# Performance work log

Measured on AMD Instinct MI355X. Metric: run time of the kernel, lower is better.

## Reference

```python
import jax, jax.numpy as jnp
import numpy as np

L, P, B, C, H, W = 2, 2, 4, 128, 64, 64
K = 2  # negatives per sample


def setup_inputs() -> dict:
    key = jax.random.key(0)
    k1, k2, k3, k4, k5 = jax.random.split(key, 5)
    shp = (L, P, B, C, H, W)
    return {
        "style_E": jax.random.normal(k1, shp, dtype=jnp.float32),
        "style_S": jax.random.normal(k2, shp, dtype=jnp.float32),
        "translate_E": jax.random.normal(k3, shp, dtype=jnp.float32),
        "translate_S": jax.random.normal(k4, shp, dtype=jnp.float32),
        "neg_idx": jax.random.randint(k5, (B, K), 0, B, dtype=jnp.int32),
    }


def reference(style_E, style_S, translate_E, translate_S, neg_idx):
    # Stack E and S levels: [2L, P, B, C, N] with N = H*W
    S = jnp.concatenate([style_E, style_S], axis=0).reshape(2 * L, P, B, C, -1)
    T = jnp.concatenate([translate_E, translate_S], axis=0).reshape(2 * L, P, B, C, -1)

    # EFDM: sort style values; permute them to trans's rank order, then MSE.
    Vs = jnp.sort(S, axis=-1)                      # value_style
    idx_t = jnp.argsort(T, axis=-1)                # index_trans
    inv = jnp.argsort(idx_t, axis=-1)              # inverse_index

    # Positive pairs: style[b] vs trans[b]
    matched_pos = jnp.take_along_axis(Vs, inv, axis=-1)
    # mse over (C, N) per slice (matches mse_loss on a [1,C,N] tensor)
    pos = jnp.mean((T - matched_pos) ** 2, axis=(3, 4))  # [2L, P, B]
    poss_loss = pos.sum(axis=(0, 1))                      # [B]

    # Negatives: style[nb] vs trans[b] for nb in neg_idx[b]
    Vs_neg = Vs[:, :, neg_idx]                            # [2L, P, B, K, C, N]
    matched_neg = jnp.take_along_axis(Vs_neg, inv[:, :, :, None], axis=-1)
    neg = jnp.mean((T[:, :, :, None] - matched_neg) ** 2, axis=(4, 5))  # [2L, P, B, K]
    neg_loss = neg.sum(axis=(0, 1, 3))                    # [B]

    return jnp.sum(poss_loss / neg_loss)
```

## Files before the change

### kernel.cpp

```cpp
#include <hip/hip_runtime.h>


typedef unsigned int u32;
typedef __fp16 f16x2 __attribute__((ext_vector_type(2)));

constexpr int N     = 4096;
constexpr int NTH   = 256;
constexpr int CDIM  = 128;
constexpr int BDIM  = 4;
constexpr int KNEG  = 2;
constexpr int ROWS  = 4096;
constexpr int HALF  = 2048;
constexpr int ROWW  = N / 2;
constexpr int LSTRW = 20;
constexpr int LDSW  = NTH * LSTRW;

__device__ inline int lslot(int t) { return t * LSTRW; }

__device__ inline u32 pk_min(u32 a, u32 b) {
  u32 d; asm("v_pk_min_f16 %0, %1, %2" : "=v"(d) : "v"(a), "v"(b)); return d;
}
__device__ inline u32 pk_max(u32 a, u32 b) {
  u32 d; asm("v_pk_max_f16 %0, %1, %2" : "=v"(d) : "v"(a), "v"(b)); return d;
}
__device__ inline u32 pk_min_negb(u32 a, u32 b) {
  u32 d; asm("v_pk_min_f16 %0, %1, %2 neg_lo:[0,1] neg_hi:[0,1]" : "=v"(d) : "v"(a), "v"(b)); return d;
}
__device__ inline u32 pk_sub(u32 a, u32 b) {
  u32 d; asm("v_pk_add_f16 %0, %1, %2 neg_lo:[0,1] neg_hi:[0,1]" : "=v"(d) : "v"(a), "v"(b)); return d;
}
__device__ inline float dot2acc(u32 d, float acc) {
  asm("v_dot2_f32_f16 %0, %1, %2, %0" : "+v"(acc) : "v"(d), "v"(d)); return acc;
}
__device__ inline void pk_cswap(u32& a, u32& b) {
  const u32 mn = pk_min(a, b), mx = pk_max(a, b);
  a = mn; b = mx;
}

template<int CTRL>
__device__ inline u32 dpp_u(u32 x) {
  return (u32)__builtin_amdgcn_update_dpp((int)x, (int)x, CTRL, 0xF, 0xF, false);
}
template<int TM>
__device__ inline u32 dppx(u32 x) {
  if constexpr (TM == 1)      return dpp_u<0xB1>(x);
  else if constexpr (TM == 2) return dpp_u<0x4E>(x);
  else if constexpr (TM == 4)
    return (u32)__builtin_amdgcn_ds_swizzle((int)x, 0x101F);
  else                        return dpp_u<0x128>(x);
}
__device__ inline void swap32u(u32& a, u32& b) {
  asm("v_permlane32_swap_b32 %0, %1" : "+v"(a), "+v"(b));
}
__device__ inline void swap16u(u32& a, u32& b) {
  asm("v_permlane16_swap_b32 %0, %1" : "+v"(a), "+v"(b));
}

__device__ inline void flip16(u32 h[16], u32 f) {
  #pragma unroll
  for (int p = 0; p < 16; ++p) h[p] ^= f;
}

struct PolM { u32 s1, s2, s4, s8; };

template<int TM>
__device__ inline void polar_pass16(u32 h[16]) {
  #pragma unroll
  for (int g = 0; g < 16; g += 8) {
    u32 o[8];
    #pragma unroll
    for (int p = 0; p < 8; ++p) o[p] = dppx<TM>(h[g + p]);
    #pragma unroll
    for (int p = 0; p < 8; ++p) h[g + p] = pk_min_negb(h[g + p], o[p]);
  }
}

template<int TMS, bool SKIP_ENTRY>
__device__ inline void polar_block16(u32 h[16], const PolM& pm) {
  if constexpr (!SKIP_ENTRY) {
    const u32 e = (TMS == 8) ? pm.s8 : (TMS == 4) ? pm.s4 : (TMS == 2) ? pm.s2 : pm.s1;
    flip16(h, e);
  }
  if constexpr (TMS >= 8) { polar_pass16<8>(h); flip16(h, pm.s8 ^ pm.s4); }
  if constexpr (TMS >= 4) { polar_pass16<4>(h); flip16(h, pm.s4 ^ pm.s2); }
  if constexpr (TMS >= 2) { polar_pass16<2>(h); flip16(h, pm.s2 ^ pm.s1); }
  polar_pass16<1>(h);
  flip16(h, pm.s1);
}

template<bool IS32>
__device__ inline void pass_perm16(u32 h[16]) {
  #pragma unroll
  for (int q = 0; q < 8; ++q) {
    u32 a = h[2*q], b = h[2*q + 1];
    if constexpr (IS32) swap32u(a, b); else swap16u(a, b);
    u32 mn = pk_min(a, b);
    u32 mx = pk_max(a, b);
    if constexpr (IS32) swap32u(mn, mx); else swap16u(mn, mx);
    h[2*q] = mn; h[2*q + 1] = mx;
  }
}

template<int TM>
__device__ inline void pass_lds16(u32 h[16], u32* buf, int t) {
  __syncthreads();
  uint4* wp = (uint4*)(buf + lslot(t));
  wp[0] = make_uint4(h[0],  h[1],  h[2],  h[3]);
  wp[1] = make_uint4(h[4],  h[5],  h[6],  h[7]);
  wp[2] = make_uint4(h[8],  h[9],  h[10], h[11]);
  wp[3] = make_uint4(h[12], h[13], h[14], h[15]);
  __syncthreads();
  const uint4* rp = (const uint4*)(buf + lslot(t ^ TM));
  const uint4 x0 = rp[0], x1 = rp[1], x2 = rp[2], x3 = rp[3];
  if (t & TM) {
    h[0]  = pk_max(h[0],  x0.x); h[1]  = pk_max(h[1],  x0.y);
    h[2]  = pk_max(h[2],  x0.z); h[3]  = pk_max(h[3],  x0.w);
    h[4]  = pk_max(h[4],  x1.x); h[5]  = pk_max(h[5],  x1.y);
    h[6]  = pk_max(h[6],  x1.z); h[7]  = pk_max(h[7],  x1.w);
    h[8]  = pk_max(h[8],  x2.x); h[9]  = pk_max(h[9],  x2.y);
    h[10] = pk_max(h[10], x2.z); h[11] = pk_max(h[11], x2.w);
    h[12] = pk_max(h[12], x3.x); h[13] = pk_max(h[13], x3.y);
    h[14] = pk_max(h[14], x3.z); h[15] = pk_max(h[15], x3.w);
  } else {
    h[0]  = pk_min(h[0],  x0.x); h[1]  = pk_min(h[1],  x0.y);
    h[2]  = pk_min(h[2],  x0.z); h[3]  = pk_min(h[3],  x0.w);
    h[4]  = pk_min(h[4],  x1.x); h[5]  = pk_min(h[5],  x1.y);
    h[6]  = pk_min(h[6],  x1.z); h[7]  = pk_min(h[7],  x1.w);
    h[8]  = pk_min(h[8],  x2.x); h[9]  = pk_min(h[9],  x2.y);
    h[10] = pk_min(h[10], x2.z); h[11] = pk_min(h[11], x2.w);
    h[12] = pk_min(h[12], x3.x); h[13] = pk_min(h[13], x3.y);
    h[14] = pk_min(h[14], x3.z); h[15] = pk_min(h[15], x3.w);
  }
}

template<int K, int J>
__device__ inline void local_pass16(u32 h[16]) {
  #pragma unroll
  for (int p = 0; p < 16; ++p)
    if ((p & J) == 0) {
      if ((p & K) == 0) pk_cswap(h[p], h[p ^ J]);
      else              pk_cswap(h[p ^ J], h[p]);
    }
}

__device__ inline void tail16(u32 h[16]) {
  #pragma unroll
  for (int p = 0; p < 16; ++p) if ((p & 8) == 0) pk_cswap(h[p], h[p ^ 8]);
  #pragma unroll
  for (int p = 0; p < 16; ++p) if ((p & 4) == 0) pk_cswap(h[p], h[p ^ 4]);
  #pragma unroll
  for (int p = 0; p < 16; ++p) if ((p & 2) == 0) pk_cswap(h[p], h[p ^ 2]);
  #pragma unroll
  for (int p = 0; p < 16; ++p) if ((p & 1) == 0) pk_cswap(h[p], h[p ^ 1]);
}

template<int K>
__device__ inline void stage16(u32 h[16], u32* buf, int t, u32& cur, const PolM& pm) {
  constexpr bool FOLD = (K >= 32 && K <= 256);
  const u32 f = (K >= 4096) ? 0u : ((t & (K >> 4)) ? 0x80008000u : 0u);
  u32 m = f ^ cur;
  if constexpr (FOLD)
    m ^= (K == 256) ? pm.s8 : (K == 128) ? pm.s4 : (K == 64) ? pm.s2 : pm.s1;
  flip16(h, m);
  cur = f;
  if constexpr (K >= 4096) pass_lds16<128>(h, buf, t);
  if constexpr (K >= 2048) pass_lds16<64>(h, buf, t);
  if constexpr (K >= 1024) pass_perm16<true>(h);
  if constexpr (K >= 512)  pass_perm16<false>(h);
  if constexpr (K >= 256)      polar_block16<8, FOLD>(h, pm);
  else if constexpr (K >= 128) polar_block16<4, FOLD>(h, pm);
  else if constexpr (K >= 64)  polar_block16<2, FOLD>(h, pm);
  else if constexpr (K >= 32)  polar_block16<1, FOLD>(h, pm);
  tail16(h);
}

__global__ __launch_bounds__(NTH)
void sort_pair(const float* __restrict__ sE, const float* __restrict__ sS,
               const float* __restrict__ tE, const float* __restrict__ tS,
               u32* __restrict__ Ss, u32* __restrict__ Ts) {
  __shared__ u32 buf[LDSW];
  const int t = threadIdx.x, r = blockIdx.x;
  const float* srcS = (r < HALF) ? sE + (size_t)r * N : sS + (size_t)(r - HALF) * N;
  const float* srcT = (r < HALF) ? tE + (size_t)r * N : tS + (size_t)(r - HALF) * N;

  u32 h[16];
  {
    const float4* a4 = (const float4*)srcS;
    const float4* b4 = (const float4*)srcT;
    #pragma unroll
    for (int q = 0; q < 4; ++q) {
      const float4 xa = a4[t*4 + q];
      const float4 xb = b4[t*4 + q];
      const f16x2 p0 = __builtin_amdgcn_cvt_pkrtz(xa.x, xb.x);
      const f16x2 p1 = __builtin_amdgcn_cvt_pkrtz(xa.y, xb.y);
      const f16x2 p2 = __builtin_amdgcn_cvt_pkrtz(xa.z, xb.z);
      const f16x2 p3 = __builtin_amdgcn_cvt_pkrtz(xa.w, xb.w);
      h[q*4+0] = __builtin_bit_cast(u32, p0);
      h[q*4+1] = __builtin_bit_cast(u32, p1);
      h[q*4+2] = __builtin_bit_cast(u32, p2);
      h[q*4+3] = __builtin_bit_cast(u32, p3);
    }
  }

  local_pass16<2, 1>(h);
  local_pass16<4, 2>(h); local_pass16<4, 1>(h);
  local_pass16<8, 4>(h); local_pass16<8, 2>(h); local_pass16<8, 1>(h);

  const u32 S = 0x80008000u;
  PolM pm;
  pm.s1 = (t & 1) ? S : 0u;  pm.s2 = (t & 2) ? S : 0u;
  pm.s4 = (t & 4) ? S : 0u;  pm.s8 = (t & 8) ? S : 0u;

  u32 cur = 0;
  stage16<16>(h, buf, t, cur, pm);
  stage16<32>(h, buf, t, cur, pm);
  stage16<64>(h, buf, t, cur, pm);
  stage16<128>(h, buf, t, cur, pm);
  stage16<256>(h, buf, t, cur, pm);
  stage16<512>(h, buf, t, cur, pm);
  stage16<1024>(h, buf, t, cur, pm);
  stage16<2048>(h, buf, t, cur, pm);
  stage16<4096>(h, buf, t, cur, pm);

  u32 A[8], B[8];
  #pragma unroll
  for (int q = 0; q < 8; ++q) {
    A[q] = __builtin_amdgcn_perm(h[2*q+1], h[2*q], 0x05040100u);
    B[q] = __builtin_amdgcn_perm(h[2*q+1], h[2*q], 0x07060302u);
  }
  uint4* dA = (uint4*)(Ss + (size_t)r * ROWW);
  uint4* dB = (uint4*)(Ts + (size_t)r * ROWW);
  dA[t]       = make_uint4(A[0], A[1], A[2], A[3]);
  dA[NTH + t] = make_uint4(A[4], A[5], A[6], A[7]);
  dB[t]       = make_uint4(B[0], B[1], B[2], B[3]);
  dB[NTH + t] = make_uint4(B[4], B[5], B[6], B[7]);
}

__global__ __launch_bounds__(NTH)
void diff_rows(const u32* __restrict__ Ss, const u32* __restrict__ Ts,
               const int* __restrict__ neg_idx, float2* __restrict__ partial) {
  __shared__ float red[2][4];
  const int t = threadIdx.x, r = blockIdx.x;

  const uint4* tp = (const uint4*)(Ts + (size_t)r * ROWW);
  const uint4 h0 = tp[t], h1 = tp[NTH + t];

  const int c  = r & (CDIM - 1);
  const int b  = (r / CDIM) & (BDIM - 1);
  const int ap = r / (CDIM * BDIM);

  float posp = 0.f, negp = 0.f;
  {
    const uint4* vp = (const uint4*)(Ss + (size_t)r * ROWW);
    const uint4 w0 = vp[t], w1 = vp[NTH + t];
    posp = dot2acc(pk_sub(h0.x, w0.x), posp);
    posp = dot2acc(pk_sub(h0.y, w0.y), posp);
    posp = dot2acc(pk_sub(h0.z, w0.z), posp);
    posp = dot2acc(pk_sub(h0.w, w0.w), posp);
    posp = dot2acc(pk_sub(h1.x, w1.x), posp);
    posp = dot2acc(pk_sub(h1.y, w1.y), posp);
    posp = dot2acc(pk_sub(h1.z, w1.z), posp);
    posp = dot2acc(pk_sub(h1.w, w1.w), posp);
  }
  #pragma unroll
  for (int k = 0; k < KNEG; ++k) {
    const int nb = neg_idx[b * KNEG + k];
    const uint4* vp = (const uint4*)(Ss + ((size_t)(ap * BDIM + nb) * CDIM + c) * ROWW);
    const uint4 w0 = vp[t], w1 = vp[NTH + t];
    negp = dot2acc(pk_sub(h0.x, w0.x), negp);
    negp = dot2acc(pk_sub(h0.y, w0.y), negp);
    negp = dot2acc(pk_sub(h0.z, w0.z), negp);
    negp = dot2acc(pk_sub(h0.w, w0.w), negp);
    negp = dot2acc(pk_sub(h1.x, w1.x), negp);
    negp = dot2acc(pk_sub(h1.y, w1.y), negp);
    negp = dot2acc(pk_sub(h1.z, w1.z), negp);
    negp = dot2acc(pk_sub(h1.w, w1.w), negp);
  }

  #pragma unroll
  for (int off = 32; off > 0; off >>= 1) {
    posp += __shfl_down(posp, off, 64);
    negp += __shfl_down(negp, off, 64);
  }
  const int wid = t >> 6, lane = t & 63;
  if (lane == 0) { red[0][wid] = posp; red[1][wid] = negp; }
  __syncthreads();
  if (t == 0) {
    const float pt = red[0][0] + red[0][1] + red[0][2] + red[0][3];
    const float nt = red[1][0] + red[1][1] + red[1][2] + red[1][3];
    partial[r] = make_float2(pt, nt);
  }
}

__global__ __launch_bounds__(NTH)
void finalize(const float2* __restrict__ partial, float* __restrict__ out) {
  __shared__ double rp[4], rn[4];
  const int t = threadIdx.x;
  const int wid = t >> 6, lane = t & 63;
  double res = 0.0;
  #pragma unroll
  for (int b = 0; b < BDIM; ++b) {
    double p = 0.0, n = 0.0;
    for (int idx = t; idx < 1024; idx += NTH) {
      const int a = idx >> 7, c = idx & 127;
      const float2 v = partial[a * 512 + b * 128 + c];
      p += (double)v.x; n += (double)v.y;
    }
    #pragma unroll
    for (int off = 32; off > 0; off >>= 1) {
      p += __shfl_down(p, off, 64);
      n += __shfl_down(n, off, 64);
    }
    if (lane == 0) { rp[wid] = p; rn[wid] = n; }
    __syncthreads();
    if (t == 0) {
      const double P = rp[0] + rp[1] + rp[2] + rp[3];
      const double Nn = rn[0] + rn[1] + rn[2] + rn[3];
      res += P / Nn;
    }
    __syncthreads();
  }
  if (t == 0) out[0] = (float)res;
}

extern "C" void kernel_launch(void* const* d_in, const int* in_sizes, int n_in,
                              void* d_out, int out_size, void* d_ws, size_t ws_size,
                              hipStream_t stream) {
  const float* style_E = (const float*)d_in[0];
  const float* style_S = (const float*)d_in[1];
  const float* trans_E = (const float*)d_in[2];
  const float* trans_S = (const float*)d_in[3];
  const int*   neg_idx = (const int*)d_in[4];

  u32*    Ss      = (u32*)d_ws;
  u32*    Ts      = Ss + (size_t)ROWS * ROWW;
  float2* partial = (float2*)(Ts + (size_t)ROWS * ROWW);

  sort_pair<<<ROWS, NTH, 0, stream>>>(style_E, style_S, trans_E, trans_S, Ss, Ts);
  diff_rows<<<ROWS, NTH, 0, stream>>>(Ss, Ts, neg_idx, partial);
  finalize<<<1, NTH, 0, stream>>>(partial, (float*)d_out);
}
```

Baseline: 104.1 us.

## Fuse positive-pair MSE into sort kernel and remap diff_rows block order

The positive-pair squared-difference reduction now runs inside sort_pair on the in-register sorted halves, so diff_rows no longer rereads the row's own sorted style data. diff_rows only computes the negative-pair terms, and its block index is remapped so that consecutive blocks are spread across the eight (level,pair) groups, which may improve L2 reuse of the gathered negative rows. The cost is an extra block reduction and sync at the end of the sort kernel.

```diff
diff --git a/kernel.cpp b/kernel.cpp
--- a/kernel.cpp
+++ b/kernel.cpp
@@ -177,7 +177,8 @@
 __global__ __launch_bounds__(NTH)
 void sort_pair(const float* __restrict__ sE, const float* __restrict__ sS,
                const float* __restrict__ tE, const float* __restrict__ tS,
-               u32* __restrict__ Ss, u32* __restrict__ Ts) {
+               u32* __restrict__ Ss, u32* __restrict__ Ts,
+               float* __restrict__ pospart) {
   __shared__ u32 buf[LDSW];
   const int t = threadIdx.x, r = blockIdx.x;
   const float* srcS = (r < HALF) ? sE + (size_t)r * N : sS + (size_t)(r - HALF) * N;
@@ -234,13 +235,27 @@
   dA[NTH + t] = make_uint4(A[4], A[5], A[6], A[7]);
   dB[t]       = make_uint4(B[0], B[1], B[2], B[3]);
   dB[NTH + t] = make_uint4(B[4], B[5], B[6], B[7]);
+
+  float posp = 0.f;
+  #pragma unroll
+  for (int q = 0; q < 8; ++q) posp = dot2acc(pk_sub(B[q], A[q]), posp);
+  #pragma unroll
+  for (int off = 32; off > 0; off >>= 1) posp += __shfl_down(posp, off, 64);
+  __syncthreads();
+  float* fred = (float*)buf;
+  const int wid = t >> 6, lane = t & 63;
+  if (lane == 0) fred[wid] = posp;
+  __syncthreads();
+  if (t == 0) pospart[r] = fred[0] + fred[1] + fred[2] + fred[3];
 }
 
 __global__ __launch_bounds__(NTH)
 void diff_rows(const u32* __restrict__ Ss, const u32* __restrict__ Ts,
-               const int* __restrict__ neg_idx, float2* __restrict__ partial) {
-  __shared__ float red[2][4];
-  const int t = threadIdx.x, r = blockIdx.x;
+               const int* __restrict__ neg_idx, float* __restrict__ negpart) {
+  __shared__ float red[4];
+  const int t = threadIdx.x;
+  const int bid = blockIdx.x;
+  const int r = ((bid & 7) << 9) + (bid >> 3);
 
   const uint4* tp = (const uint4*)(Ts + (size_t)r * ROWW);
   const uint4 h0 = tp[t], h1 = tp[NTH + t];
@@ -249,19 +264,7 @@
   const int b  = (r / CDIM) & (BDIM - 1);
   const int ap = r / (CDIM * BDIM);
 
-  float posp = 0.f, negp = 0.f;
-  {
-    const uint4* vp = (const uint4*)(Ss + (size_t)r * ROWW);
-    const uint4 w0 = vp[t], w1 = vp[NTH + t];
-    posp = dot2acc(pk_sub(h0.x, w0.x), posp);
-    posp = dot2acc(pk_sub(h0.y, w0.y), posp);
-    posp = dot2acc(pk_sub(h0.z, w0.z), posp);
-    posp = dot2acc(pk_sub(h0.w, w0.w), posp);
-    posp = dot2acc(pk_sub(h1.x, w1.x), posp);
-    posp = dot2acc(pk_sub(h1.y, w1.y), posp);
-    posp = dot2acc(pk_sub(h1.z, w1.z), posp);
-    posp = dot2acc(pk_sub(h1.w, w1.w), posp);
-  }
+  float negp = 0.f;
   #pragma unroll
   for (int k = 0; k < KNEG; ++k) {
     const int nb = neg_idx[b * KNEG + k];
@@ -278,22 +281,16 @@
   }
 
   #pragma unroll
-  for (int off = 32; off > 0; off >>= 1) {
-    posp += __shfl_down(posp, off, 64);
-    negp += __shfl_down(negp, off, 64);
-  }
+  for (int off = 32; off > 0; off >>= 1) negp += __shfl_down(negp, off, 64);
   const int wid = t >> 6, lane = t & 63;
-  if (lane == 0) { red[0][wid] = posp; red[1][wid] = negp; }
-  __syncthreads();
-  if (t == 0) {
-    const float pt = red[0][0] + red[0][1] + red[0][2] + red[0][3];
-    const float nt = red[1][0] + red[1][1] + red[1][2] + red[1][3];
-    partial[r] = make_float2(pt, nt);
-  }
+  if (lane == 0) red[wid] = negp;
+  __syncthreads();
+  if (t == 0) negpart[r] = red[0] + red[1] + red[2] + red[3];
 }
 
 __global__ __launch_bounds__(NTH)
-void finalize(const float2* __restrict__ partial, float* __restrict__ out) {
+void finalize(const float* __restrict__ pospart, const float* __restrict__ negpart,
+              float* __restrict__ out) {
   __shared__ double rp[4], rn[4];
   const int t = threadIdx.x;
   const int wid = t >> 6, lane = t & 63;
@@ -303,8 +300,9 @@
     double p = 0.0, n = 0.0;
     for (int idx = t; idx < 1024; idx += NTH) {
       const int a = idx >> 7, c = idx & 127;
-      const float2 v = partial[a * 512 + b * 128 + c];
-      p += (double)v.x; n += (double)v.y;
+      const int rr = a * 512 + b * 128 + c;
+      p += (double)pospart[rr];
+      n += (double)negpart[rr];
     }
     #pragma unroll
     for (int off = 32; off > 0; off >>= 1) {
@@ -332,11 +330,12 @@
   const float* trans_S = (const float*)d_in[3];
   const int*   neg_idx = (const int*)d_in[4];
 
-  u32*    Ss      = (u32*)d_ws;
-  u32*    Ts      = Ss + (size_t)ROWS * ROWW;
-  float2* partial = (float2*)(Ts + (size_t)ROWS * ROWW);
-
-  sort_pair<<<ROWS, NTH, 0, stream>>>(style_E, style_S, trans_E, trans_S, Ss, Ts);
-  diff_rows<<<ROWS, NTH, 0, stream>>>(Ss, Ts, neg_idx, partial);
-  finalize<<<1, NTH, 0, stream>>>(partial, (float*)d_out);
-}
+  u32*   Ss      = (u32*)d_ws;
+  u32*   Ts      = Ss + (size_t)ROWS * ROWW;
+  float* pospart = (float*)(Ts + (size_t)ROWS * ROWW);
+  float* negpart = pospart + ROWS;
+
+  sort_pair<<<ROWS, NTH, 0, stream>>>(style_E, style_S, trans_E, trans_S, Ss, Ts, pospart);
+  diff_rows<<<ROWS, NTH, 0, stream>>>(Ss, Ts, neg_idx, negpart);
+  finalize<<<1, NTH, 0, stream>>>(pospart, negpart, (float*)d_out);
+}
```

New measurement: 105.2 us. Within noise of the previous version (+1.1%).
